# Kernel tuning notes

Hardware: AMD Instinct MI355X
Metric: run time of the kernel (lower is better)

The kernel has to match this reference:

```python
import jax, jax.numpy as jnp
import numpy as np

N_NODES = 50000
N_EDGES = 400000
HID = 128
D_EDGE = 3
D_OUT = 3
LN_EPS = 1e-5


def silu(x):
    return x * jax.nn.sigmoid(x)


def layer_norm(x, gamma, beta):
    mu = jnp.mean(x, axis=-1, keepdims=True)
    var = jnp.mean(jnp.square(x - mu), axis=-1, keepdims=True)
    return (x - mu) * jax.lax.rsqrt(var + LN_EPS) * gamma + beta


def ffn(x, W1, b1, W2, b2, act, gamma=None, beta=None):
    # Linear -> act -> Linear, optional final LayerNorm (FeedForwardBlock)
    h = act(x @ W1 + b1)
    y = h @ W2 + b2
    if gamma is not None:
        y = layer_norm(y, gamma, beta)
    return y


def _mlp_params(key, d_in, d_hid, d_out, use_ln):
    ks = jax.random.split(key, 4)
    p = {
        'W1': jax.random.normal(ks[0], (d_in, d_hid), jnp.float32) / np.sqrt(d_in),
        'b1': jnp.zeros((d_hid,), jnp.float32),
        'W2': jax.random.normal(ks[1], (d_hid, d_out), jnp.float32) / np.sqrt(d_hid),
        'b2': jnp.zeros((d_out,), jnp.float32),
    }
    if use_ln:
        p['g'] = jnp.ones((d_out,), jnp.float32)
        p['be'] = jnp.zeros((d_out,), jnp.float32)
    return p


def setup_inputs() -> dict:
    key = jax.random.key(0)
    ks = jax.random.split(key, 8)
    edge_idx = jax.random.randint(ks[0], (N_EDGES, 2), 0, N_NODES, dtype=jnp.int64)
    edge_features = jax.random.normal(ks[1], (N_EDGES, D_EDGE), jnp.float32)
    node_latents = jax.random.normal(ks[2], (N_NODES, HID), jnp.float32)
    node_features = jax.random.normal(ks[3], (N_NODES, HID), jnp.float32)
    ee = _mlp_params(ks[4], D_EDGE, HID, HID, True)            # embed_edge_fn
    pe = _mlp_params(ks[5], 3 * HID, HID, HID, True)           # process_edge_fn
    pn = _mlp_params(ks[6], 2 * HID, HID, HID, True)           # process_node_fn
    no = _mlp_params(ks[7], HID, HID, D_OUT, False)            # node_output_fn
    inp = {'edge_idx': edge_idx, 'edge_features': edge_features,
           'node_latents': node_latents, 'node_features': node_features}
    for tag, p in (('ee', ee), ('pe', pe), ('pn', pn), ('no', no)):
        for k, v in p.items():
            inp[f'{tag}_{k}'] = v
    return inp


def reference(edge_idx, edge_features, node_latents, node_features,
              ee_W1, ee_b1, ee_W2, ee_b2, ee_g, ee_be,
              pe_W1, pe_b1, pe_W2, pe_b2, pe_g, pe_be,
              pn_W1, pn_b1, pn_W2, pn_b2, pn_g, pn_be,
              no_W1, no_b1, no_W2, no_b2):
    n_nodes = node_features.shape[0]
    senders = edge_idx[:, 0]
    receivers = edge_idx[:, 1]

    # embed raw edge features: [E, D_EDGE] -> [E, HID]
    edge_lat = ffn(edge_features, ee_W1, ee_b1, ee_W2, ee_b2, silu, ee_g, ee_be)

    # edge update: gather sender latents / receiver features, concat-MLP
    sender_f = node_latents[senders]       # [E, HID]
    receiver_f = node_features[receivers]  # [E, HID]
    e_in = jnp.concatenate([sender_f, receiver_f, edge_lat], axis=-1)  # [E, 3*HID]
    new_edge = ffn(e_in, pe_W1, pe_b1, pe_W2, pe_b2, silu, pe_g, pe_be)

    # node update: scatter-mean over receivers, concat-MLP
    seg_sum = jax.ops.segment_sum(new_edge, receivers, num_segments=n_nodes)
    cnt = jax.ops.segment_sum(jnp.ones((new_edge.shape[0], 1), new_edge.dtype),
                              receivers, num_segments=n_nodes)
    mean_edges = seg_sum / jnp.maximum(cnt, 1.0)
    n_in = jnp.concatenate([node_features, mean_edges], axis=-1)  # [N, 2*HID]
    new_node = ffn(n_in, pn_W1, pn_b1, pn_W2, pn_b2, silu, pn_g, pn_be)

    # output head (sigmoid hidden activation, no layer norm)
    out = ffn(new_node, no_W1, no_b1, no_W2, no_b2, jax.nn.sigmoid)
    return (edge_lat, out)
```

## Files before the change

### kernel.cpp

```cpp
#include <hip/hip_runtime.h>


#define N_NODES 50000
#define N_EDGES 400000
#define HID 128
#define LN_EPS 1e-5f

typedef unsigned short u16;
typedef __attribute__((ext_vector_type(8))) short short8;
typedef __attribute__((ext_vector_type(4))) float floatx4;

__device__ __forceinline__ u16 f2bf(float f) {
    union { float f; unsigned int i; } v; v.f = f;
    unsigned int x = v.i;
    return (u16)((x + 0x7FFFu + ((x >> 16) & 1u)) >> 16);
}
__device__ __forceinline__ float bf2f(u16 u) {
    union { unsigned int i; float f; } v; v.i = ((unsigned int)u) << 16;
    return v.f;
}
__device__ __forceinline__ float siluf(float x) { return x * (1.0f / (1.0f + __expf(-x))); }
__device__ __forceinline__ float sigmf(float x) { return 1.0f / (1.0f + __expf(-x)); }

__device__ __forceinline__ short8 pack8(const float* __restrict__ p) {
    union { u16 u[8]; short8 v; } o;
    float4 a = *(const float4*)p;
    float4 b = *(const float4*)(p + 4);
    o.u[0] = f2bf(a.x); o.u[1] = f2bf(a.y); o.u[2] = f2bf(a.z); o.u[3] = f2bf(a.w);
    o.u[4] = f2bf(b.x); o.u[5] = f2bf(b.y); o.u[6] = f2bf(b.z); o.u[7] = f2bf(b.w);
    return o.v;
}
__device__ __forceinline__ short8 pack8s(const float* __restrict__ p, float sc) {
    union { u16 u[8]; short8 v; } o;
    float4 a = *(const float4*)p;
    float4 b = *(const float4*)(p + 4);
    o.u[0] = f2bf(a.x * sc); o.u[1] = f2bf(a.y * sc); o.u[2] = f2bf(a.z * sc); o.u[3] = f2bf(a.w * sc);
    o.u[4] = f2bf(b.x * sc); o.u[5] = f2bf(b.y * sc); o.u[6] = f2bf(b.z * sc); o.u[7] = f2bf(b.w * sc);
    return o.v;
}

__device__ __forceinline__ char* swzp(const void* base, int row, int b) {
    return (char*)base + row * 256 + ((b & 15) | ((((b >> 4) ^ row) & 15) << 4));
}
__device__ __forceinline__ char* swz64(const void* base, int row, int b) {
    return (char*)base + row * 128 + ((b & 15) | ((((b >> 4) ^ row) & 7) << 4));
}

__global__ void k_prepT(const float* __restrict__ src, u16* __restrict__ dst, int K, int N) {
    int i = blockIdx.x * blockDim.x + threadIdx.x;
    if (i < K * N) {
        int k = i / N, n = i - k * N;
        dst[n * K + k] = f2bf(src[i]);
    }
}

__launch_bounds__(256)
__global__ void k_edge_ee(const float* __restrict__ ef,
                          const float* __restrict__ W1, const float* __restrict__ b1v,
                          const u16* __restrict__ W2T, const float* __restrict__ b2v,
                          const float* __restrict__ g, const float* __restrict__ be,
                          float* __restrict__ outEL, u16* __restrict__ elB) {
    __shared__ __align__(16) u16 sW2[128 * 136];
    __shared__ float sW1[384];
    __shared__ float sB1[128];
    const int t = threadIdx.x;
    const int lane = t & 63, w = t >> 6;
    const int l15 = lane & 15, quad = lane >> 4;

    for (int i = t; i < 2048; i += 256) {
        int n = i >> 4, q = i & 15;
        *(uint4*)&sW2[n * 136 + q * 8] = *(const uint4*)&W2T[n * 128 + q * 8];
    }
    for (int i = t; i < 384; i += 256) sW1[i] = W1[i];
    if (t < 128) sB1[t] = b1v[t];
    __syncthreads();

    float b2r[8], gr[8], ber[8];
    #pragma unroll
    for (int nt = 0; nt < 8; ++nt) {
        int col = nt * 16 + l15;
        b2r[nt] = b2v[col]; gr[nt] = g[col]; ber[nt] = be[col];
    }

    for (int tile = blockIdx.x; tile < N_EDGES / 64; tile += gridDim.x) {
        const int e0 = tile * 64;
        const int em = e0 + w * 16 + l15;
        float f0 = ef[em * 3 + 0], f1 = ef[em * 3 + 1], f2 = ef[em * 3 + 2];
        short8 ha[4];
        #pragma unroll
        for (int ks = 0; ks < 4; ++ks) {
            union { u16 u[8]; short8 v; } hh;
            #pragma unroll
            for (int jj = 0; jj < 8; ++jj) {
                int j = ks * 32 + quad * 8 + jj;
                float x = sB1[j] + f0 * sW1[j] + f1 * sW1[128 + j] + f2 * sW1[256 + j];
                hh.u[jj] = f2bf(siluf(x));
            }
            ha[ks] = hh.v;
        }
        floatx4 acc[8];
        #pragma unroll
        for (int nt = 0; nt < 8; ++nt) acc[nt] = (floatx4){0.f, 0.f, 0.f, 0.f};
        #pragma unroll
        for (int ks = 0; ks < 4; ++ks) {
            #pragma unroll
            for (int nt = 0; nt < 8; ++nt) {
                short8 bv = *(const short8*)&sW2[(nt * 16 + l15) * 136 + ks * 32 + quad * 8];
                acc[nt] = __builtin_amdgcn_mfma_f32_16x16x32_bf16(ha[ks], bv, acc[nt], 0, 0, 0);
            }
        }
        float sum[4] = {0, 0, 0, 0}, sq[4] = {0, 0, 0, 0};
        #pragma unroll
        for (int nt = 0; nt < 8; ++nt)
            #pragma unroll
            for (int rr = 0; rr < 4; ++rr) {
                float v = acc[nt][rr] + b2r[nt];
                acc[nt][rr] = v; sum[rr] += v; sq[rr] += v * v;
            }
        #pragma unroll
        for (int m = 1; m < 16; m <<= 1)
            #pragma unroll
            for (int rr = 0; rr < 4; ++rr) {
                sum[rr] += __shfl_xor(sum[rr], m);
                sq[rr]  += __shfl_xor(sq[rr], m);
            }
        float mu[4], rs[4];
        #pragma unroll
        for (int rr = 0; rr < 4; ++rr) {
            mu[rr] = sum[rr] * (1.0f / HID);
            float var = fmaxf(sq[rr] * (1.0f / HID) - mu[rr] * mu[rr], 0.f);
            rs[rr] = rsqrtf(var + LN_EPS);
        }
        #pragma unroll
        for (int nt = 0; nt < 8; ++nt) {
            int col = nt * 16 + l15;
            #pragma unroll
            for (int rr = 0; rr < 4; ++rr) {
                int row = e0 + w * 16 + quad * 4 + rr;
                float v = (acc[nt][rr] - mu[rr]) * rs[rr] * gr[nt] + ber[nt];
                outEL[(size_t)row * HID + col] = v;
                if (elB) elB[(size_t)row * HID + col] = f2bf(v);
            }
        }
    }
}

__launch_bounds__(256)
__global__ void k_gemm128(const float* __restrict__ A, const u16* __restrict__ WT,
                          int ldw, int koff, u16* __restrict__ out) {
    __shared__ __align__(16) u16 sW[128 * 128];
    const int t = threadIdx.x;
    const int lane = t & 63, w = t >> 6;
    const int l15 = lane & 15, quad = lane >> 4;
    for (int i = t; i < 2048; i += 256) {
        int n = i >> 4, q = i & 15;
        *(uint4*)swzp(sW, n, q * 16) = *(const uint4*)&WT[n * ldw + koff + q * 8];
    }
    __syncthreads();
    const int NT = (N_NODES + 63) / 64;
    for (int tile = blockIdx.x; tile < NT; tile += gridDim.x) {
        const int n0 = tile * 64;
        const int arow = n0 + w * 16 + l15;
        const int ac = arow < N_NODES ? arow : 0;
        short8 a[4];
        #pragma unroll
        for (int ks = 0; ks < 4; ++ks)
            a[ks] = pack8(&A[(size_t)ac * HID + ks * 32 + quad * 8]);
        floatx4 acc[8];
        #pragma unroll
        for (int nt = 0; nt < 8; ++nt) acc[nt] = (floatx4){0.f, 0.f, 0.f, 0.f};
        #pragma unroll
        for (int ks = 0; ks < 4; ++ks)
            #pragma unroll
            for (int nt = 0; nt < 8; ++nt) {
                short8 bv = *(const short8*)swzp(sW, nt * 16 + l15, ks * 64 + quad * 16);
                acc[nt] = __builtin_amdgcn_mfma_f32_16x16x32_bf16(a[ks], bv, acc[nt], 0, 0, 0);
            }
        #pragma unroll
        for (int nt = 0; nt < 8; ++nt) {
            #pragma unroll
            for (int rr = 0; rr < 4; ++rr) {
                int orow = n0 + w * 16 + quad * 4 + rr;
                if (orow < N_NODES)
                    out[(size_t)orow * HID + l15 * 8 + nt] = f2bf(acc[nt][rr]);
            }
        }
    }
}

template<bool ELB>
__launch_bounds__(512, 4)
__global__ void k_edge_pe(const int* __restrict__ eidx,
                          const u16* __restrict__ P1, const u16* __restrict__ P2,
                          const float* __restrict__ el, const u16* __restrict__ elB,
                          const u16* __restrict__ W1T, const float* __restrict__ b1v,
                          const u16* __restrict__ W2T, const float* __restrict__ b2v,
                          const float* __restrict__ g, const float* __restrict__ be,
                          float* __restrict__ seg, float* __restrict__ cnt) {
    __shared__ __align__(16) u16 sW1[128 * 128];
    __shared__ __align__(16) u16 sW2[128 * 128];
    __shared__ __align__(16) u16 sH[8][16 * 64];
    const int t = threadIdx.x;
    const int lane = t & 63, w = t >> 6;
    const int l15 = lane & 15, quad = lane >> 4;

    for (int i = t; i < 2048; i += 512) {
        int n = i >> 4, q = i & 15;
        *(uint4*)swzp(sW1, n, q * 16) = *(const uint4*)&W1T[n * 384 + 256 + q * 8];
        *(uint4*)swzp(sW2, n, q * 16) = *(const uint4*)&W2T[n * 128 + q * 8];
    }
    float b1r[8], b2r[8], gr[8], ber[8];
    #pragma unroll
    for (int nt = 0; nt < 8; ++nt) {
        int col = nt * 16 + l15;
        b1r[nt] = b1v[col]; b2r[nt] = b2v[col]; gr[nt] = g[col]; ber[nt] = be[col];
    }
    __syncthreads();

    for (int tile = blockIdx.x; tile < N_EDGES / 128; tile += gridDim.x) {
        const int e0 = tile * 128;
        const int em = e0 + w * 16 + l15;
        int snd[4], rcv[4];
        #pragma unroll
        for (int rr = 0; rr < 4; ++rr) {
            int e = e0 + w * 16 + quad * 4 + rr;
            int2 p = *(const int2*)&eidx[e * 2];
            snd[rr] = p.x; rcv[rr] = p.y;
        }
        floatx4 acc[8];
        #pragma unroll
        for (int rr = 0; rr < 4; ++rr) {
            union { u16 u[8]; short8 v; } p1, p2;
            p1.v = *(const short8*)&P1[(size_t)snd[rr] * HID + l15 * 8];
            p2.v = *(const short8*)&P2[(size_t)rcv[rr] * HID + l15 * 8];
            #pragma unroll
            for (int nt = 0; nt < 8; ++nt)
                acc[nt][rr] = b1r[nt] + bf2f(p1.u[nt]) + bf2f(p2.u[nt]);
        }
        short8 a[4];
        #pragma unroll
        for (int ks = 0; ks < 4; ++ks) {
            if (ELB) a[ks] = *(const short8*)&elB[(size_t)em * HID + ks * 32 + quad * 8];
            else     a[ks] = pack8(&el[(size_t)em * HID + ks * 32 + quad * 8]);
        }
        #pragma unroll
        for (int ks = 0; ks < 4; ++ks)
            #pragma unroll
            for (int nt = 0; nt < 8; ++nt) {
                short8 bv = *(const short8*)swzp(sW1, nt * 16 + l15, ks * 64 + quad * 16);
                acc[nt] = __builtin_amdgcn_mfma_f32_16x16x32_bf16(a[ks], bv, acc[nt], 0, 0, 0);
            }
        short8 ha[4];
        #pragma unroll
        for (int ph = 0; ph < 2; ++ph) {
            #pragma unroll
            for (int n4 = 0; n4 < 4; ++n4) {
                int nt = ph * 4 + n4;
                #pragma unroll
                for (int rr = 0; rr < 4; ++rr)
                    *(u16*)swz64(sH[w], quad * 4 + rr, (n4 * 16 + l15) * 2) =
                        f2bf(siluf(acc[nt][rr]));
            }
            #pragma unroll
            for (int k2 = 0; k2 < 2; ++k2)
                ha[ph * 2 + k2] = *(const short8*)swz64(sH[w], l15, k2 * 64 + quad * 16);
        }
        floatx4 acc2[8];
        #pragma unroll
        for (int nt = 0; nt < 8; ++nt) acc2[nt] = (floatx4){0.f, 0.f, 0.f, 0.f};
        #pragma unroll
        for (int ks = 0; ks < 4; ++ks)
            #pragma unroll
            for (int nt = 0; nt < 8; ++nt) {
                short8 bv = *(const short8*)swzp(sW2, nt * 16 + l15, ks * 64 + quad * 16);
                acc2[nt] = __builtin_amdgcn_mfma_f32_16x16x32_bf16(ha[ks], bv, acc2[nt], 0, 0, 0);
            }
        float sum[4] = {0, 0, 0, 0}, sq[4] = {0, 0, 0, 0};
        #pragma unroll
        for (int nt = 0; nt < 8; ++nt)
            #pragma unroll
            for (int rr = 0; rr < 4; ++rr) {
                float v = acc2[nt][rr] + b2r[nt];
                acc2[nt][rr] = v; sum[rr] += v; sq[rr] += v * v;
            }
        #pragma unroll
        for (int m = 1; m < 16; m <<= 1)
            #pragma unroll
            for (int rr = 0; rr < 4; ++rr) {
                sum[rr] += __shfl_xor(sum[rr], m);
                sq[rr]  += __shfl_xor(sq[rr], m);
            }
        float mu[4], rs[4];
        #pragma unroll
        for (int rr = 0; rr < 4; ++rr) {
            mu[rr] = sum[rr] * (1.0f / HID);
            float var = fmaxf(sq[rr] * (1.0f / HID) - mu[rr] * mu[rr], 0.f);
            rs[rr] = rsqrtf(var + LN_EPS);
        }
        #pragma unroll
        for (int nt = 0; nt < 8; ++nt) {
            int col = nt * 16 + l15;
            #pragma unroll
            for (int rr = 0; rr < 4; ++rr) {
                float v = (acc2[nt][rr] - mu[rr]) * rs[rr] * gr[nt] + ber[nt];
                atomicAdd(&seg[(size_t)rcv[rr] * HID + col], v);
            }
        }
        if (l15 == 0) {
            #pragma unroll
            for (int rr = 0; rr < 4; ++rr) atomicAdd(&cnt[rcv[rr]], 1.0f);
        }
    }
}

__launch_bounds__(512, 4)
__global__ void k_node(const u16* __restrict__ Q1,
                       const float* __restrict__ seg, const float* __restrict__ cnt,
                       const u16* __restrict__ W1T, const float* __restrict__ b1v,
                       const u16* __restrict__ W2T, const float* __restrict__ b2v,
                       const float* __restrict__ g, const float* __restrict__ be,
                       const u16* __restrict__ noW1T, const float* __restrict__ nob1,
                       const float* __restrict__ noW2, const float* __restrict__ nob2,
                       float* __restrict__ outN) {
    __shared__ __align__(16) u16 sW1[128 * 128];
    __shared__ __align__(16) u16 sW2[128 * 128];
    __shared__ __align__(16) u16 sH[8][16 * 64];
    const int t = threadIdx.x;
    const int lane = t & 63, w = t >> 6;
    const int l15 = lane & 15, quad = lane >> 4;

    for (int i = t; i < 2048; i += 512) {
        int n = i >> 4, q = i & 15;
        *(uint4*)swzp(sW1, n, q * 16) = *(const uint4*)&W1T[n * 256 + 128 + q * 8];
        *(uint4*)swzp(sW2, n, q * 16) = *(const uint4*)&W2T[n * 128 + q * 8];
    }
    float b1r[8], b2r[8], gr[8], ber[8], nob1r[8], w2r[8][3];
    #pragma unroll
    for (int nt = 0; nt < 8; ++nt) {
        int col = nt * 16 + l15;
        b1r[nt] = b1v[col]; b2r[nt] = b2v[col]; gr[nt] = g[col]; ber[nt] = be[col];
        nob1r[nt] = nob1[col];
        #pragma unroll
        for (int c = 0; c < 3; ++c) w2r[nt][c] = noW2[col * 3 + c];
    }
    float nob2r[3] = {nob2[0], nob2[1], nob2[2]};
    __syncthreads();

    const int NT = (N_NODES + 127) / 128;
    for (int tile = blockIdx.x; tile < NT; tile += gridDim.x) {
        const int n0 = tile * 128;
        const int node = n0 + w * 16 + l15;
        const int nc = node < N_NODES ? node : 0;
        float inv = 1.0f / fmaxf(cnt[nc], 1.0f);
        short8 a[4];
        #pragma unroll
        for (int ks = 0; ks < 4; ++ks)
            a[ks] = pack8s(&seg[(size_t)nc * HID + ks * 32 + quad * 8], inv);
        floatx4 acc[8];
        int crow[4];
        #pragma unroll
        for (int rr = 0; rr < 4; ++rr) {
            int r = n0 + w * 16 + quad * 4 + rr;
            crow[rr] = r;
            r = r < N_NODES ? r : 0;
            union { u16 u[8]; short8 v; } q1;
            q1.v = *(const short8*)&Q1[(size_t)r * HID + l15 * 8];
            #pragma unroll
            for (int nt = 0; nt < 8; ++nt)
                acc[nt][rr] = b1r[nt] + bf2f(q1.u[nt]);
        }
        #pragma unroll
        for (int ks = 0; ks < 4; ++ks)
            #pragma unroll
            for (int nt = 0; nt < 8; ++nt) {
                short8 bv = *(const short8*)swzp(sW1, nt * 16 + l15, ks * 64 + quad * 16);
                acc[nt] = __builtin_amdgcn_mfma_f32_16x16x32_bf16(a[ks], bv, acc[nt], 0, 0, 0);
            }
        short8 ha[4];
        #pragma unroll
        for (int ph = 0; ph < 2; ++ph) {
            #pragma unroll
            for (int n4 = 0; n4 < 4; ++n4) {
                int nt = ph * 4 + n4;
                #pragma unroll
                for (int rr = 0; rr < 4; ++rr)
                    *(u16*)swz64(sH[w], quad * 4 + rr, (n4 * 16 + l15) * 2) =
                        f2bf(siluf(acc[nt][rr]));
            }
            #pragma unroll
            for (int k2 = 0; k2 < 2; ++k2)
                ha[ph * 2 + k2] = *(const short8*)swz64(sH[w], l15, k2 * 64 + quad * 16);
        }
        floatx4 acc2[8];
        #pragma unroll
        for (int nt = 0; nt < 8; ++nt) acc2[nt] = (floatx4){0.f, 0.f, 0.f, 0.f};
        #pragma unroll
        for (int ks = 0; ks < 4; ++ks)
            #pragma unroll
            for (int nt = 0; nt < 8; ++nt) {
                short8 bv = *(const short8*)swzp(sW2, nt * 16 + l15, ks * 64 + quad * 16);
                acc2[nt] = __builtin_amdgcn_mfma_f32_16x16x32_bf16(ha[ks], bv, acc2[nt], 0, 0, 0);
            }
        float sum[4] = {0, 0, 0, 0}, sq[4] = {0, 0, 0, 0};
        #pragma unroll
        for (int nt = 0; nt < 8; ++nt)
            #pragma unroll
            for (int rr = 0; rr < 4; ++rr) {
                float v = acc2[nt][rr] + b2r[nt];
                acc2[nt][rr] = v; sum[rr] += v; sq[rr] += v * v;
            }
        #pragma unroll
        for (int m = 1; m < 16; m <<= 1)
            #pragma unroll
            for (int rr = 0; rr < 4; ++rr) {
                sum[rr] += __shfl_xor(sum[rr], m);
                sq[rr]  += __shfl_xor(sq[rr], m);
            }
        float mu[4], rs[4];
        #pragma unroll
        for (int rr = 0; rr < 4; ++rr) {
            mu[rr] = sum[rr] * (1.0f / HID);
            float var = fmaxf(sq[rr] * (1.0f / HID) - mu[rr] * mu[rr], 0.f);
            rs[rr] = rsqrtf(var + LN_EPS);
        }
        short8 h2[4];
        #pragma unroll
        for (int ph = 0; ph < 2; ++ph) {
            #pragma unroll
            for (int n4 = 0; n4 < 4; ++n4) {
                int nt = ph * 4 + n4;
                #pragma unroll
                for (int rr = 0; rr < 4; ++rr)
                    *(u16*)swz64(sH[w], quad * 4 + rr, (n4 * 16 + l15) * 2) =
                        f2bf((acc2[nt][rr] - mu[rr]) * rs[rr] * gr[nt] + ber[nt]);
            }
            #pragma unroll
            for (int k2 = 0; k2 < 2; ++k2)
                h2[ph * 2 + k2] = *(const short8*)swz64(sH[w], l15, k2 * 64 + quad * 16);
        }
        floatx4 acc3[8];
        #pragma unroll
        for (int nt = 0; nt < 8; ++nt) acc3[nt] = (floatx4){0.f, 0.f, 0.f, 0.f};
        #pragma unroll
        for (int ks = 0; ks < 4; ++ks)
            #pragma unroll
            for (int nt = 0; nt < 8; ++nt) {
                short8 bv = *(const short8*)&noW1T[(size_t)(nt * 16 + l15) * 128 +
                                                   ks * 32 + quad * 8];
                acc3[nt] = __builtin_amdgcn_mfma_f32_16x16x32_bf16(h2[ks], bv, acc3[nt], 0, 0, 0);
            }
        float p[4][3] = {{0,0,0},{0,0,0},{0,0,0},{0,0,0}};
        #pragma unroll
        for (int nt = 0; nt < 8; ++nt)
            #pragma unroll
            for (int rr = 0; rr < 4; ++rr) {
                float h3 = sigmf(acc3[nt][rr] + nob1r[nt]);
                #pragma unroll
                for (int c = 0; c < 3; ++c) p[rr][c] += h3 * w2r[nt][c];
            }
        #pragma unroll
        for (int m = 1; m < 16; m <<= 1)
            #pragma unroll
            for (int rr = 0; rr < 4; ++rr)
                #pragma unroll
                for (int c = 0; c < 3; ++c) p[rr][c] += __shfl_xor(p[rr][c], m);
        if (l15 < 3) {
            #pragma unroll
            for (int rr = 0; rr < 4; ++rr)
                if (crow[rr] < N_NODES)
                    outN[(size_t)crow[rr] * 3 + l15] = p[rr][l15] + nob2r[l15];
        }
    }
}

extern "C" void kernel_launch(void* const* d_in, const int* in_sizes, int n_in,
                              void* d_out, int out_size, void* d_ws, size_t ws_size,
                              hipStream_t stream) {
    const int*   eidx  = (const int*)d_in[0];
    const float* ef    = (const float*)d_in[1];
    const float* nlat  = (const float*)d_in[2];
    const float* nfeat = (const float*)d_in[3];
    const float* eeW1 = (const float*)d_in[4];
    const float* eeb1 = (const float*)d_in[5];
    const float* eeW2 = (const float*)d_in[6];
    const float* eeb2 = (const float*)d_in[7];
    const float* eeg  = (const float*)d_in[8];
    const float* eebe = (const float*)d_in[9];
    const float* peW1 = (const float*)d_in[10];
    const float* peb1 = (const float*)d_in[11];
    const float* peW2 = (const float*)d_in[12];
    const float* peb2 = (const float*)d_in[13];
    const float* peg  = (const float*)d_in[14];
    const float* pebe = (const float*)d_in[15];
    const float* pnW1 = (const float*)d_in[16];
    const float* pnb1 = (const float*)d_in[17];
    const float* pnW2 = (const float*)d_in[18];
    const float* pnb2 = (const float*)d_in[19];
    const float* png_ = (const float*)d_in[20];
    const float* pnbe = (const float*)d_in[21];
    const float* noW1 = (const float*)d_in[22];
    const float* nob1 = (const float*)d_in[23];
    const float* noW2 = (const float*)d_in[24];
    const float* nob2 = (const float*)d_in[25];

    char* ws = (char*)d_ws;
    float* seg = (float*)ws;
    float* cnt = (float*)(ws + 25600000);
    u16* eeW2T = (u16*)(ws + 25800000);
    u16* peW1T = (u16*)(ws + 25832768);
    u16* peW2T = (u16*)(ws + 25931072);
    u16* pnW1T = (u16*)(ws + 25963840);
    u16* pnW2T = (u16*)(ws + 26029376);
    u16* noW1T = (u16*)(ws + 26062144);
    u16* P1    = (u16*)(ws + 26094912);
    u16* P2    = (u16*)(ws + 38894912);
    const size_t WS_ELB = 51694912 + (size_t)N_EDGES * HID * 2;
    u16* elB = (ws_size >= WS_ELB) ? (u16*)(ws + 51694912) : (u16*)nullptr;

    hipMemsetAsync(ws, 0, 25800000, stream);

    k_prepT<<<64, 256, 0, stream>>>(eeW2, eeW2T, 128, 128);
    k_prepT<<<192, 256, 0, stream>>>(peW1, peW1T, 384, 128);
    k_prepT<<<64, 256, 0, stream>>>(peW2, peW2T, 128, 128);
    k_prepT<<<128, 256, 0, stream>>>(pnW1, pnW1T, 256, 128);
    k_prepT<<<64, 256, 0, stream>>>(pnW2, pnW2T, 128, 128);
    k_prepT<<<64, 256, 0, stream>>>(noW1, noW1T, 128, 128);

    float* outEL = (float*)d_out;
    float* outN  = outEL + (size_t)N_EDGES * HID;

    k_edge_ee<<<1024, 256, 0, stream>>>(ef, eeW1, eeb1, eeW2T, eeb2, eeg, eebe,
                                        outEL, elB);
    k_gemm128<<<512, 256, 0, stream>>>(nlat,  peW1T, 384, 0,   P1);
    k_gemm128<<<512, 256, 0, stream>>>(nfeat, peW1T, 384, 128, P2);
    if (elB)
        k_edge_pe<true><<<512, 512, 0, stream>>>(eidx, P1, P2, outEL, elB, peW1T, peb1,
                                                 peW2T, peb2, peg, pebe, seg, cnt);
    else
        k_edge_pe<false><<<512, 512, 0, stream>>>(eidx, P1, P2, outEL, elB, peW1T, peb1,
                                                  peW2T, peb2, peg, pebe, seg, cnt);
    k_gemm128<<<512, 256, 0, stream>>>(nfeat, pnW1T, 256, 0, P1);
    k_node<<<391, 512, 0, stream>>>(P1, seg, cnt, pnW1T, pnb1, pnW2T, pnb2, png_, pnbe,
                                    noW1T, nob1, noW2, nob2, outN);
}
```

Measured before the change: 773.8 us.

## Replace atomic scatter-mean with CSR gather over bf16 edge outputs

Builds a receiver-sorted CSR index each call (histogram, single-block scan, atomic fill). The edge kernel now writes new edge latents as bf16 via a shared-memory transpose instead of doing float atomics into a node-sized accumulator, and a new per-node kernel gathers and averages them into a bf16 mean. This removes the large memset and the contended float atomics, but adds CSR build kernels, a 100MB edge buffer write and read, and drops the bf16 copy of the edge embedding. k_gemm128 output stores are also vectorised to 16-byte writes.

```diff
diff --git a/kernel.cpp b/kernel.cpp
--- a/kernel.cpp
+++ b/kernel.cpp
@@ -54,12 +54,54 @@
     }
 }
 
+__global__ void k_hist(const int* __restrict__ eidx, int* __restrict__ icnt) {
+    int e = blockIdx.x * blockDim.x + threadIdx.x;
+    if (e < N_EDGES) atomicAdd(&icnt[eidx[e * 2 + 1]], 1);
+}
+
+__launch_bounds__(1024)
+__global__ void k_scan(const int* __restrict__ icnt, int* __restrict__ offs) {
+    __shared__ int s[1024];
+    const int t = threadIdx.x;
+    const int CH = 49;
+    int base = t * CH;
+    int sum = 0;
+    for (int j = 0; j < CH; ++j) {
+        int i = base + j;
+        if (i < N_NODES) sum += icnt[i];
+    }
+    s[t] = sum;
+    __syncthreads();
+    for (int off = 1; off < 1024; off <<= 1) {
+        int v = (t >= off) ? s[t - off] : 0;
+        __syncthreads();
+        s[t] += v;
+        __syncthreads();
+    }
+    int run = s[t] - sum;
+    for (int j = 0; j < CH; ++j) {
+        int i = base + j;
+        if (i < N_NODES) { offs[i] = run; run += icnt[i]; }
+    }
+    if (t == 1023) offs[N_NODES] = s[1023];
+}
+
+__global__ void k_fill(const int* __restrict__ eidx, const int* __restrict__ offs,
+                       int* __restrict__ fpos, int* __restrict__ csr) {
+    int e = blockIdx.x * blockDim.x + threadIdx.x;
+    if (e < N_EDGES) {
+        int r = eidx[e * 2 + 1];
+        int p = atomicAdd(&fpos[r], 1);
+        csr[offs[r] + p] = e;
+    }
+}
+
 __launch_bounds__(256)
 __global__ void k_edge_ee(const float* __restrict__ ef,
                           const float* __restrict__ W1, const float* __restrict__ b1v,
                           const u16* __restrict__ W2T, const float* __restrict__ b2v,
                           const float* __restrict__ g, const float* __restrict__ be,
-                          float* __restrict__ outEL, u16* __restrict__ elB) {
+                          float* __restrict__ outEL) {
     __shared__ __align__(16) u16 sW2[128 * 136];
     __shared__ float sW1[384];
     __shared__ float sB1[128];
@@ -137,9 +179,7 @@
             #pragma unroll
             for (int rr = 0; rr < 4; ++rr) {
                 int row = e0 + w * 16 + quad * 4 + rr;
-                float v = (acc[nt][rr] - mu[rr]) * rs[rr] * gr[nt] + ber[nt];
-                outEL[(size_t)row * HID + col] = v;
-                if (elB) elB[(size_t)row * HID + col] = f2bf(v);
+                outEL[(size_t)row * HID + col] = (acc[nt][rr] - mu[rr]) * rs[rr] * gr[nt] + ber[nt];
             }
         }
     }
@@ -177,25 +217,26 @@
                 acc[nt] = __builtin_amdgcn_mfma_f32_16x16x32_bf16(a[ks], bv, acc[nt], 0, 0, 0);
             }
         #pragma unroll
-        for (int nt = 0; nt < 8; ++nt) {
-            #pragma unroll
-            for (int rr = 0; rr < 4; ++rr) {
-                int orow = n0 + w * 16 + quad * 4 + rr;
-                if (orow < N_NODES)
-                    out[(size_t)orow * HID + l15 * 8 + nt] = f2bf(acc[nt][rr]);
-            }
-        }
-    }
-}
-
-template<bool ELB>
+        for (int rr = 0; rr < 4; ++rr) {
+            int orow = n0 + w * 16 + quad * 4 + rr;
+            union { u16 u[8]; short8 v; } o;
+            #pragma unroll
+            for (int nt = 0; nt < 8; ++nt) o.u[nt] = f2bf(acc[nt][rr]);
+            if (orow < N_NODES)
+                *(short8*)&out[(size_t)orow * HID + l15 * 8] = o.v;
+        }
+    }
+}
+
+template<bool CSR>
 __launch_bounds__(512, 4)
 __global__ void k_edge_pe(const int* __restrict__ eidx,
                           const u16* __restrict__ P1, const u16* __restrict__ P2,
-                          const float* __restrict__ el, const u16* __restrict__ elB,
+                          const float* __restrict__ el,
                           const u16* __restrict__ W1T, const float* __restrict__ b1v,
                           const u16* __restrict__ W2T, const float* __restrict__ b2v,
                           const float* __restrict__ g, const float* __restrict__ be,
+                          u16* __restrict__ newE,
                           float* __restrict__ seg, float* __restrict__ cnt) {
     __shared__ __align__(16) u16 sW1[128 * 128];
     __shared__ __align__(16) u16 sW2[128 * 128];
@@ -239,10 +280,8 @@
         }
         short8 a[4];
         #pragma unroll
-        for (int ks = 0; ks < 4; ++ks) {
-            if (ELB) a[ks] = *(const short8*)&elB[(size_t)em * HID + ks * 32 + quad * 8];
-            else     a[ks] = pack8(&el[(size_t)em * HID + ks * 32 + quad * 8]);
-        }
+        for (int ks = 0; ks < 4; ++ks)
+            a[ks] = pack8(&el[(size_t)em * HID + ks * 32 + quad * 8]);
         #pragma unroll
         for (int ks = 0; ks < 4; ++ks)
             #pragma unroll
@@ -297,24 +336,66 @@
             float var = fmaxf(sq[rr] * (1.0f / HID) - mu[rr] * mu[rr], 0.f);
             rs[rr] = rsqrtf(var + LN_EPS);
         }
-        #pragma unroll
-        for (int nt = 0; nt < 8; ++nt) {
-            int col = nt * 16 + l15;
-            #pragma unroll
-            for (int rr = 0; rr < 4; ++rr) {
-                float v = (acc2[nt][rr] - mu[rr]) * rs[rr] * gr[nt] + ber[nt];
-                atomicAdd(&seg[(size_t)rcv[rr] * HID + col], v);
-            }
-        }
-        if (l15 == 0) {
-            #pragma unroll
-            for (int rr = 0; rr < 4; ++rr) atomicAdd(&cnt[rcv[rr]], 1.0f);
-        }
-    }
-}
-
+        if (CSR) {
+            #pragma unroll
+            for (int ph = 0; ph < 2; ++ph) {
+                #pragma unroll
+                for (int n4 = 0; n4 < 4; ++n4) {
+                    int nt = ph * 4 + n4;
+                    #pragma unroll
+                    for (int rr = 0; rr < 4; ++rr)
+                        *(u16*)swz64(sH[w], quad * 4 + rr, (n4 * 16 + l15) * 2) =
+                            f2bf((acc2[nt][rr] - mu[rr]) * rs[rr] * gr[nt] + ber[nt]);
+                }
+                #pragma unroll
+                for (int k2 = 0; k2 < 2; ++k2) {
+                    short8 row = *(const short8*)swz64(sH[w], l15, k2 * 64 + quad * 16);
+                    *(short8*)&newE[(size_t)em * HID + ph * 64 + k2 * 32 + quad * 8] = row;
+                }
+            }
+        } else {
+            #pragma unroll
+            for (int nt = 0; nt < 8; ++nt) {
+                int col = nt * 16 + l15;
+                #pragma unroll
+                for (int rr = 0; rr < 4; ++rr) {
+                    float v = (acc2[nt][rr] - mu[rr]) * rs[rr] * gr[nt] + ber[nt];
+                    atomicAdd(&seg[(size_t)rcv[rr] * HID + col], v);
+                }
+            }
+            if (l15 == 0) {
+                #pragma unroll
+                for (int rr = 0; rr < 4; ++rr) atomicAdd(&cnt[rcv[rr]], 1.0f);
+            }
+        }
+    }
+}
+
+__launch_bounds__(256)
+__global__ void k_mean(const u16* __restrict__ newE, const int* __restrict__ offs,
+                       const int* __restrict__ csr, u16* __restrict__ meanB) {
+    const int wid = (int)((blockIdx.x * blockDim.x + threadIdx.x) >> 6);
+    const int lane = threadIdx.x & 63;
+    const int nW = (int)((gridDim.x * blockDim.x) >> 6);
+    for (int n = wid; n < N_NODES; n += nW) {
+        int s0 = offs[n], s1 = offs[n + 1];
+        float a0 = 0.f, a1 = 0.f;
+        for (int d = s0; d < s1; ++d) {
+            int e = csr[d];
+            unsigned int v = *(const unsigned int*)&newE[(size_t)e * HID + lane * 2];
+            a0 += bf2f((u16)(v & 0xFFFFu));
+            a1 += bf2f((u16)(v >> 16));
+        }
+        int deg = s1 - s0;
+        float inv = 1.0f / (float)(deg > 0 ? deg : 1);
+        unsigned int o = (unsigned int)f2bf(a0 * inv) | (((unsigned int)f2bf(a1 * inv)) << 16);
+        *(unsigned int*)&meanB[(size_t)n * HID + lane * 2] = o;
+    }
+}
+
+template<bool CSR>
 __launch_bounds__(512, 4)
-__global__ void k_node(const u16* __restrict__ Q1,
+__global__ void k_node(const u16* __restrict__ Q1, const u16* __restrict__ meanB,
                        const float* __restrict__ seg, const float* __restrict__ cnt,
                        const u16* __restrict__ W1T, const float* __restrict__ b1v,
                        const u16* __restrict__ W2T, const float* __restrict__ b2v,
@@ -351,11 +432,17 @@
         const int n0 = tile * 128;
         const int node = n0 + w * 16 + l15;
         const int nc = node < N_NODES ? node : 0;
-        float inv = 1.0f / fmaxf(cnt[nc], 1.0f);
         short8 a[4];
-        #pragma unroll
-        for (int ks = 0; ks < 4; ++ks)
-            a[ks] = pack8s(&seg[(size_t)nc * HID + ks * 32 + quad * 8], inv);
+        if (CSR) {
+            #pragma unroll
+            for (int ks = 0; ks < 4; ++ks)
+                a[ks] = *(const short8*)&meanB[(size_t)nc * HID + ks * 32 + quad * 8];
+        } else {
+            float inv = 1.0f / fmaxf(cnt[nc], 1.0f);
+            #pragma unroll
+            for (int ks = 0; ks < 4; ++ks)
+                a[ks] = pack8s(&seg[(size_t)nc * HID + ks * 32 + quad * 8], inv);
+        }
         floatx4 acc[8];
         int crow[4];
         #pragma unroll
@@ -503,43 +590,84 @@
     const float* noW2 = (const float*)d_in[24];
     const float* nob2 = (const float*)d_in[25];
 
-    char* ws = (char*)d_ws;
-    float* seg = (float*)ws;
-    float* cnt = (float*)(ws + 25600000);
-    u16* eeW2T = (u16*)(ws + 25800000);
-    u16* peW1T = (u16*)(ws + 25832768);
-    u16* peW2T = (u16*)(ws + 25931072);
-    u16* pnW1T = (u16*)(ws + 25963840);
-    u16* pnW2T = (u16*)(ws + 26029376);
-    u16* noW1T = (u16*)(ws + 26062144);
-    u16* P1    = (u16*)(ws + 26094912);
-    u16* P2    = (u16*)(ws + 38894912);
-    const size_t WS_ELB = 51694912 + (size_t)N_EDGES * HID * 2;
-    u16* elB = (ws_size >= WS_ELB) ? (u16*)(ws + 51694912) : (u16*)nullptr;
-
-    hipMemsetAsync(ws, 0, 25800000, stream);
-
-    k_prepT<<<64, 256, 0, stream>>>(eeW2, eeW2T, 128, 128);
-    k_prepT<<<192, 256, 0, stream>>>(peW1, peW1T, 384, 128);
-    k_prepT<<<64, 256, 0, stream>>>(peW2, peW2T, 128, 128);
-    k_prepT<<<128, 256, 0, stream>>>(pnW1, pnW1T, 256, 128);
-    k_prepT<<<64, 256, 0, stream>>>(pnW2, pnW2T, 128, 128);
-    k_prepT<<<64, 256, 0, stream>>>(noW1, noW1T, 128, 128);
-
     float* outEL = (float*)d_out;
     float* outN  = outEL + (size_t)N_EDGES * HID;
-
-    k_edge_ee<<<1024, 256, 0, stream>>>(ef, eeW1, eeb1, eeW2T, eeb2, eeg, eebe,
-                                        outEL, elB);
-    k_gemm128<<<512, 256, 0, stream>>>(nlat,  peW1T, 384, 0,   P1);
-    k_gemm128<<<512, 256, 0, stream>>>(nfeat, peW1T, 384, 128, P2);
-    if (elB)
-        k_edge_pe<true><<<512, 512, 0, stream>>>(eidx, P1, P2, outEL, elB, peW1T, peb1,
-                                                 peW2T, peb2, peg, pebe, seg, cnt);
-    else
-        k_edge_pe<false><<<512, 512, 0, stream>>>(eidx, P1, P2, outEL, elB, peW1T, peb1,
-                                                  peW2T, peb2, peg, pebe, seg, cnt);
-    k_gemm128<<<512, 256, 0, stream>>>(nfeat, pnW1T, 256, 0, P1);
-    k_node<<<391, 512, 0, stream>>>(P1, seg, cnt, pnW1T, pnb1, pnW2T, pnb2, png_, pnbe,
-                                    noW1T, nob1, noW2, nob2, outN);
-}
+    char* ws = (char*)d_ws;
+
+    const size_t WS_CSR = 130494928;
+    const bool useCSR = ws_size >= WS_CSR;
+
+    u16 *eeW2T, *peW1T, *peW2T, *pnW1T, *pnW2T, *noW1T, *P1, *P2;
+    if (useCSR) {
+        eeW2T = (u16*)(ws + 0);
+        peW1T = (u16*)(ws + 32768);
+        peW2T = (u16*)(ws + 131072);
+        pnW1T = (u16*)(ws + 163840);
+        pnW2T = (u16*)(ws + 229376);
+        noW1T = (u16*)(ws + 262144);
+        int* icnt = (int*)(ws + 294912);
+        int* offs = (int*)(ws + 494912);
+        int* fpos = (int*)(ws + 694916);
+        int* csr  = (int*)(ws + 894916);
+        P1 = (u16*)(ws + 2494928);
+        P2 = (u16*)(ws + 15294928);
+        u16* newE  = (u16*)(ws + 28094928);
+        u16* meanB = P2;
+
+        hipMemsetAsync(ws + 294912, 0, 600004, stream);
+
+        k_prepT<<<64, 256, 0, stream>>>(eeW2, eeW2T, 128, 128);
+        k_prepT<<<192, 256, 0, stream>>>(peW1, peW1T, 384, 128);
+        k_prepT<<<64, 256, 0, stream>>>(peW2, peW2T, 128, 128);
+        k_prepT<<<128, 256, 0, stream>>>(pnW1, pnW1T, 256, 128);
+        k_prepT<<<64, 256, 0, stream>>>(pnW2, pnW2T, 128, 128);
+        k_prepT<<<64, 256, 0, stream>>>(noW1, noW1T, 128, 128);
+
+        k_hist<<<782, 512, 0, stream>>>(eidx, icnt);
+        k_scan<<<1, 1024, 0, stream>>>(icnt, offs);
+        k_fill<<<782, 512, 0, stream>>>(eidx, offs, fpos, csr);
+
+        k_edge_ee<<<1024, 256, 0, stream>>>(ef, eeW1, eeb1, eeW2T, eeb2, eeg, eebe, outEL);
+        k_gemm128<<<512, 256, 0, stream>>>(nlat,  peW1T, 384, 0,   P1);
+        k_gemm128<<<512, 256, 0, stream>>>(nfeat, peW1T, 384, 128, P2);
+        k_edge_pe<true><<<512, 512, 0, stream>>>(eidx, P1, P2, outEL, peW1T, peb1,
+                                                 peW2T, peb2, peg, pebe, newE,
+                                                 (float*)nullptr, (float*)nullptr);
+        k_mean<<<1024, 256, 0, stream>>>(newE, offs, csr, meanB);
+        k_gemm128<<<512, 256, 0, stream>>>(nfeat, pnW1T, 256, 0, P1);
+        k_node<true><<<391, 512, 0, stream>>>(P1, meanB, (float*)nullptr, (float*)nullptr,
+                                              pnW1T, pnb1, pnW2T, pnb2, png_, pnbe,
+                                              noW1T, nob1, noW2, nob2, outN);
+    } else {
+        float* seg = (float*)ws;
+        float* cnt = (float*)(ws + 25600000);
+        eeW2T = (u16*)(ws + 25800000);
+        peW1T = (u16*)(ws + 25832768);
+        peW2T = (u16*)(ws + 25931072);
+        pnW1T = (u16*)(ws + 25963840);
+        pnW2T = (u16*)(ws + 26029376);
+        noW1T = (u16*)(ws + 26062144);
+        P1    = (u16*)(ws + 26094912);
+        P2    = (u16*)(ws + 38894912);
+
+        hipMemsetAsync(ws, 0, 25800000, stream);
+
+        k_prepT<<<64, 256, 0, stream>>>(eeW2, eeW2T, 128, 128);
+        k_prepT<<<192, 256, 0, stream>>>(peW1, peW1T, 384, 128);
+        k_prepT<<<64, 256, 0, stream>>>(peW2, peW2T, 128, 128);
+        k_prepT<<<128, 256, 0, stream>>>(pnW1, pnW1T, 256, 128);
+        k_prepT<<<64, 256, 0, stream>>>(pnW2, pnW2T, 128, 128);
+        k_prepT<<<64, 256, 0, stream>>>(noW1, noW1T, 128, 128);
+
+        k_edge_ee<<<1024, 256, 0, stream>>>(ef, eeW1, eeb1, eeW2T, eeb2, eeg, eebe, outEL);
+        k_gemm128<<<512, 256, 0, stream>>>(nlat,  peW1T, 384, 0,   P1);
+        k_gemm128<<<512, 256, 0, stream>>>(nfeat, peW1T, 384, 128, P2);
+        k_edge_pe<false><<<512, 512, 0, stream>>>(eidx, P1, P2, outEL, peW1T, peb1,
+                                                  peW2T, peb2, peg, pebe, (u16*)nullptr,
+                                                  seg, cnt);
+        k_gemm128<<<512, 256, 0, stream>>>(nfeat, pnW1T, 256, 0, P1);
+        k_node<false><<<391, 512, 0, stream>>>(P1, (u16*)nullptr, seg, cnt,
+                                               pnW1T, pnb1, pnW2T, pnb2, png_, pnbe,
+                                               noW1T, nob1, noW2, nob2, outN);
+    }
+}
```

Result: slower. 1.043 ms (+34.7%).

## Replace atomic scatter-mean with CSR-by-receiver per-node edge processing

Applied to the files above, without the earlier changes.

Builds a receiver-sorted CSR (histogram, single-block scan, fill) and processes edges grouped per destination node, one wave per node, so the segment mean is reduced in registers and written once as bf16. This removes the 128 float atomics per edge, the large seg/cnt memset, and the fp32 seg re-read in the node kernel. The cost is three extra small kernels, a serial one-block scan, and partly-filled 16-row MFMA tiles for low-degree nodes (average degree about 8), which roughly doubles the MFMA work for the edge MLP. The bf16 edge-latent copy is dropped, and gathers of edge latents become random rather than contiguous.

```diff
diff --git a/kernel.cpp b/kernel.cpp
--- a/kernel.cpp
+++ b/kernel.cpp
@@ -30,14 +30,6 @@
     o.u[4] = f2bf(b.x); o.u[5] = f2bf(b.y); o.u[6] = f2bf(b.z); o.u[7] = f2bf(b.w);
     return o.v;
 }
-__device__ __forceinline__ short8 pack8s(const float* __restrict__ p, float sc) {
-    union { u16 u[8]; short8 v; } o;
-    float4 a = *(const float4*)p;
-    float4 b = *(const float4*)(p + 4);
-    o.u[0] = f2bf(a.x * sc); o.u[1] = f2bf(a.y * sc); o.u[2] = f2bf(a.z * sc); o.u[3] = f2bf(a.w * sc);
-    o.u[4] = f2bf(b.x * sc); o.u[5] = f2bf(b.y * sc); o.u[6] = f2bf(b.z * sc); o.u[7] = f2bf(b.w * sc);
-    return o.v;
-}
 
 __device__ __forceinline__ char* swzp(const void* base, int row, int b) {
     return (char*)base + row * 256 + ((b & 15) | ((((b >> 4) ^ row) & 15) << 4));
@@ -54,12 +46,55 @@
     }
 }
 
+__global__ void k_hist(const int* __restrict__ eidx, int* __restrict__ icnt) {
+    int e = blockIdx.x * blockDim.x + threadIdx.x;
+    if (e < N_EDGES) atomicAdd(&icnt[eidx[e * 2 + 1]], 1);
+}
+
+__launch_bounds__(1024)
+__global__ void k_scan(const int* __restrict__ icnt, int* __restrict__ offs) {
+    __shared__ int s[1024];
+    const int t = threadIdx.x;
+    const int CH = 49;
+    int base = t * CH;
+    int sum = 0;
+    for (int j = 0; j < CH; ++j) {
+        int i = base + j;
+        if (i < N_NODES) sum += icnt[i];
+    }
+    s[t] = sum;
+    __syncthreads();
+    for (int off = 1; off < 1024; off <<= 1) {
+        int v = (t >= off) ? s[t - off] : 0;
+        __syncthreads();
+        s[t] += v;
+        __syncthreads();
+    }
+    int run = s[t] - sum;
+    for (int j = 0; j < CH; ++j) {
+        int i = base + j;
+        if (i < N_NODES) { offs[i] = run; run += icnt[i]; }
+    }
+    if (t == 1023) offs[N_NODES] = s[1023];
+}
+
+__global__ void k_fill(const int* __restrict__ eidx, const int* __restrict__ offs,
+                       int* __restrict__ fpos, int2* __restrict__ csrES) {
+    int e = blockIdx.x * blockDim.x + threadIdx.x;
+    if (e < N_EDGES) {
+        int2 pr = *(const int2*)&eidx[e * 2];
+        int p = atomicAdd(&fpos[pr.y], 1);
+        int2 es; es.x = e; es.y = pr.x;
+        csrES[offs[pr.y] + p] = es;
+    }
+}
+
 __launch_bounds__(256)
 __global__ void k_edge_ee(const float* __restrict__ ef,
                           const float* __restrict__ W1, const float* __restrict__ b1v,
                           const u16* __restrict__ W2T, const float* __restrict__ b2v,
                           const float* __restrict__ g, const float* __restrict__ be,
-                          float* __restrict__ outEL, u16* __restrict__ elB) {
+                          float* __restrict__ outEL) {
     __shared__ __align__(16) u16 sW2[128 * 136];
     __shared__ float sW1[384];
     __shared__ float sB1[128];
@@ -137,9 +172,7 @@
             #pragma unroll
             for (int rr = 0; rr < 4; ++rr) {
                 int row = e0 + w * 16 + quad * 4 + rr;
-                float v = (acc[nt][rr] - mu[rr]) * rs[rr] * gr[nt] + ber[nt];
-                outEL[(size_t)row * HID + col] = v;
-                if (elB) elB[(size_t)row * HID + col] = f2bf(v);
+                outEL[(size_t)row * HID + col] = (acc[nt][rr] - mu[rr]) * rs[rr] * gr[nt] + ber[nt];
             }
         }
     }
@@ -177,34 +210,33 @@
                 acc[nt] = __builtin_amdgcn_mfma_f32_16x16x32_bf16(a[ks], bv, acc[nt], 0, 0, 0);
             }
         #pragma unroll
-        for (int nt = 0; nt < 8; ++nt) {
-            #pragma unroll
-            for (int rr = 0; rr < 4; ++rr) {
-                int orow = n0 + w * 16 + quad * 4 + rr;
-                if (orow < N_NODES)
-                    out[(size_t)orow * HID + l15 * 8 + nt] = f2bf(acc[nt][rr]);
-            }
-        }
-    }
-}
-
-template<bool ELB>
-__launch_bounds__(512, 4)
-__global__ void k_edge_pe(const int* __restrict__ eidx,
+        for (int rr = 0; rr < 4; ++rr) {
+            int orow = n0 + w * 16 + quad * 4 + rr;
+            union { u16 u[8]; short8 v; } o;
+            #pragma unroll
+            for (int nt = 0; nt < 8; ++nt) o.u[nt] = f2bf(acc[nt][rr]);
+            if (orow < N_NODES)
+                *(short8*)&out[(size_t)orow * HID + l15 * 8] = o.v;
+        }
+    }
+}
+
+__launch_bounds__(256)
+__global__ void k_pe_node(const int2* __restrict__ csrES, const int* __restrict__ offs,
                           const u16* __restrict__ P1, const u16* __restrict__ P2,
-                          const float* __restrict__ el, const u16* __restrict__ elB,
+                          const float* __restrict__ el,
                           const u16* __restrict__ W1T, const float* __restrict__ b1v,
                           const u16* __restrict__ W2T, const float* __restrict__ b2v,
                           const float* __restrict__ g, const float* __restrict__ be,
-                          float* __restrict__ seg, float* __restrict__ cnt) {
+                          u16* __restrict__ meanB) {
     __shared__ __align__(16) u16 sW1[128 * 128];
     __shared__ __align__(16) u16 sW2[128 * 128];
-    __shared__ __align__(16) u16 sH[8][16 * 64];
+    __shared__ __align__(16) u16 sH[4][16 * 64];
     const int t = threadIdx.x;
     const int lane = t & 63, w = t >> 6;
     const int l15 = lane & 15, quad = lane >> 4;
 
-    for (int i = t; i < 2048; i += 512) {
+    for (int i = t; i < 2048; i += 256) {
         int n = i >> 4, q = i & 15;
         *(uint4*)swzp(sW1, n, q * 16) = *(const uint4*)&W1T[n * 384 + 256 + q * 8];
         *(uint4*)swzp(sW2, n, q * 16) = *(const uint4*)&W2T[n * 128 + q * 8];
@@ -217,105 +249,115 @@
     }
     __syncthreads();
 
-    for (int tile = blockIdx.x; tile < N_EDGES / 128; tile += gridDim.x) {
-        const int e0 = tile * 128;
-        const int em = e0 + w * 16 + l15;
-        int snd[4], rcv[4];
-        #pragma unroll
-        for (int rr = 0; rr < 4; ++rr) {
-            int e = e0 + w * 16 + quad * 4 + rr;
-            int2 p = *(const int2*)&eidx[e * 2];
-            snd[rr] = p.x; rcv[rr] = p.y;
-        }
-        floatx4 acc[8];
-        #pragma unroll
-        for (int rr = 0; rr < 4; ++rr) {
-            union { u16 u[8]; short8 v; } p1, p2;
-            p1.v = *(const short8*)&P1[(size_t)snd[rr] * HID + l15 * 8];
-            p2.v = *(const short8*)&P2[(size_t)rcv[rr] * HID + l15 * 8];
+    const int nW = (int)((gridDim.x * blockDim.x) >> 6);
+    const int wid = (int)((blockIdx.x * blockDim.x + threadIdx.x) >> 6);
+
+    for (int n = wid; n < N_NODES; n += nW) {
+        const int s0 = offs[n], s1 = offs[n + 1];
+        const int deg = s1 - s0;
+        float msum[8];
+        #pragma unroll
+        for (int nt = 0; nt < 8; ++nt) msum[nt] = 0.f;
+        union { u16 u[8]; short8 v; } p2r;
+        p2r.v = *(const short8*)&P2[(size_t)n * HID + l15 * 8];
+
+        for (int c0 = s0; c0 < s1; c0 += 16) {
+            int nv = s1 - c0; if (nv > 16) nv = 16;
+            int2 es = csrES[c0 + (l15 < nv ? l15 : nv - 1)];
+            short8 a[4];
+            #pragma unroll
+            for (int ks = 0; ks < 4; ++ks)
+                a[ks] = pack8(&el[(size_t)es.x * HID + ks * 32 + quad * 8]);
+            floatx4 acc[8];
+            #pragma unroll
+            for (int rr = 0; rr < 4; ++rr) {
+                int sndr = __shfl(es.y, quad * 4 + rr);
+                union { u16 u[8]; short8 v; } p1r;
+                p1r.v = *(const short8*)&P1[(size_t)sndr * HID + l15 * 8];
+                #pragma unroll
+                for (int nt = 0; nt < 8; ++nt)
+                    acc[nt][rr] = b1r[nt] + bf2f(p1r.u[nt]) + bf2f(p2r.u[nt]);
+            }
+            #pragma unroll
+            for (int ks = 0; ks < 4; ++ks)
+                #pragma unroll
+                for (int nt = 0; nt < 8; ++nt) {
+                    short8 bv = *(const short8*)swzp(sW1, nt * 16 + l15, ks * 64 + quad * 16);
+                    acc[nt] = __builtin_amdgcn_mfma_f32_16x16x32_bf16(a[ks], bv, acc[nt], 0, 0, 0);
+                }
+            short8 ha[4];
+            #pragma unroll
+            for (int ph = 0; ph < 2; ++ph) {
+                #pragma unroll
+                for (int n4 = 0; n4 < 4; ++n4) {
+                    int nt = ph * 4 + n4;
+                    #pragma unroll
+                    for (int rr = 0; rr < 4; ++rr)
+                        *(u16*)swz64(sH[w], quad * 4 + rr, (n4 * 16 + l15) * 2) =
+                            f2bf(siluf(acc[nt][rr]));
+                }
+                #pragma unroll
+                for (int k2 = 0; k2 < 2; ++k2)
+                    ha[ph * 2 + k2] = *(const short8*)swz64(sH[w], l15, k2 * 64 + quad * 16);
+            }
+            floatx4 acc2[8];
+            #pragma unroll
+            for (int nt = 0; nt < 8; ++nt) acc2[nt] = (floatx4){0.f, 0.f, 0.f, 0.f};
+            #pragma unroll
+            for (int ks = 0; ks < 4; ++ks)
+                #pragma unroll
+                for (int nt = 0; nt < 8; ++nt) {
+                    short8 bv = *(const short8*)swzp(sW2, nt * 16 + l15, ks * 64 + quad * 16);
+                    acc2[nt] = __builtin_amdgcn_mfma_f32_16x16x32_bf16(ha[ks], bv, acc2[nt], 0, 0, 0);
+                }
+            float sum[4] = {0, 0, 0, 0}, sq[4] = {0, 0, 0, 0};
             #pragma unroll
             for (int nt = 0; nt < 8; ++nt)
-                acc[nt][rr] = b1r[nt] + bf2f(p1.u[nt]) + bf2f(p2.u[nt]);
-        }
-        short8 a[4];
-        #pragma unroll
-        for (int ks = 0; ks < 4; ++ks) {
-            if (ELB) a[ks] = *(const short8*)&elB[(size_t)em * HID + ks * 32 + quad * 8];
-            else     a[ks] = pack8(&el[(size_t)em * HID + ks * 32 + quad * 8]);
-        }
-        #pragma unroll
-        for (int ks = 0; ks < 4; ++ks)
+                #pragma unroll
+                for (int rr = 0; rr < 4; ++rr) {
+                    float v = acc2[nt][rr] + b2r[nt];
+                    acc2[nt][rr] = v; sum[rr] += v; sq[rr] += v * v;
+                }
+            #pragma unroll
+            for (int m = 1; m < 16; m <<= 1)
+                #pragma unroll
+                for (int rr = 0; rr < 4; ++rr) {
+                    sum[rr] += __shfl_xor(sum[rr], m);
+                    sq[rr]  += __shfl_xor(sq[rr], m);
+                }
+            float mu[4], rs[4];
+            #pragma unroll
+            for (int rr = 0; rr < 4; ++rr) {
+                mu[rr] = sum[rr] * (1.0f / HID);
+                float var = fmaxf(sq[rr] * (1.0f / HID) - mu[rr] * mu[rr], 0.f);
+                rs[rr] = rsqrtf(var + LN_EPS);
+            }
             #pragma unroll
             for (int nt = 0; nt < 8; ++nt) {
-                short8 bv = *(const short8*)swzp(sW1, nt * 16 + l15, ks * 64 + quad * 16);
-                acc[nt] = __builtin_amdgcn_mfma_f32_16x16x32_bf16(a[ks], bv, acc[nt], 0, 0, 0);
-            }
-        short8 ha[4];
-        #pragma unroll
-        for (int ph = 0; ph < 2; ++ph) {
-            #pragma unroll
-            for (int n4 = 0; n4 < 4; ++n4) {
-                int nt = ph * 4 + n4;
-                #pragma unroll
-                for (int rr = 0; rr < 4; ++rr)
-                    *(u16*)swz64(sH[w], quad * 4 + rr, (n4 * 16 + l15) * 2) =
-                        f2bf(siluf(acc[nt][rr]));
-            }
-            #pragma unroll
-            for (int k2 = 0; k2 < 2; ++k2)
-                ha[ph * 2 + k2] = *(const short8*)swz64(sH[w], l15, k2 * 64 + quad * 16);
-        }
-        floatx4 acc2[8];
-        #pragma unroll
-        for (int nt = 0; nt < 8; ++nt) acc2[nt] = (floatx4){0.f, 0.f, 0.f, 0.f};
-        #pragma unroll
-        for (int ks = 0; ks < 4; ++ks)
-            #pragma unroll
-            for (int nt = 0; nt < 8; ++nt) {
-                short8 bv = *(const short8*)swzp(sW2, nt * 16 + l15, ks * 64 + quad * 16);
-                acc2[nt] = __builtin_amdgcn_mfma_f32_16x16x32_bf16(ha[ks], bv, acc2[nt], 0, 0, 0);
-            }
-        float sum[4] = {0, 0, 0, 0}, sq[4] = {0, 0, 0, 0};
-        #pragma unroll
-        for (int nt = 0; nt < 8; ++nt)
-            #pragma unroll
-            for (int rr = 0; rr < 4; ++rr) {
-                float v = acc2[nt][rr] + b2r[nt];
-                acc2[nt][rr] = v; sum[rr] += v; sq[rr] += v * v;
-            }
-        #pragma unroll
-        for (int m = 1; m < 16; m <<= 1)
-            #pragma unroll
-            for (int rr = 0; rr < 4; ++rr) {
-                sum[rr] += __shfl_xor(sum[rr], m);
-                sq[rr]  += __shfl_xor(sq[rr], m);
-            }
-        float mu[4], rs[4];
-        #pragma unroll
-        for (int rr = 0; rr < 4; ++rr) {
-            mu[rr] = sum[rr] * (1.0f / HID);
-            float var = fmaxf(sq[rr] * (1.0f / HID) - mu[rr] * mu[rr], 0.f);
-            rs[rr] = rsqrtf(var + LN_EPS);
-        }
-        #pragma unroll
-        for (int nt = 0; nt < 8; ++nt) {
-            int col = nt * 16 + l15;
-            #pragma unroll
-            for (int rr = 0; rr < 4; ++rr) {
-                float v = (acc2[nt][rr] - mu[rr]) * rs[rr] * gr[nt] + ber[nt];
-                atomicAdd(&seg[(size_t)rcv[rr] * HID + col], v);
-            }
-        }
-        if (l15 == 0) {
-            #pragma unroll
-            for (int rr = 0; rr < 4; ++rr) atomicAdd(&cnt[rcv[rr]], 1.0f);
-        }
+                float s = 0.f;
+                #pragma unroll
+                for (int rr = 0; rr < 4; ++rr) {
+                    float v = (acc2[nt][rr] - mu[rr]) * rs[rr] * gr[nt] + ber[nt];
+                    if (quad * 4 + rr < nv) s += v;
+                }
+                s += __shfl_xor(s, 16);
+                s += __shfl_xor(s, 32);
+                msum[nt] += s;
+            }
+        }
+        float inv = 1.0f / (float)(deg > 0 ? deg : 1);
+        u16* sm = (u16*)sH[w];
+        if (quad == 0) {
+            #pragma unroll
+            for (int nt = 0; nt < 8; ++nt) sm[nt * 16 + l15] = f2bf(msum[nt] * inv);
+        }
+        if (quad == 0)
+            *(short8*)&meanB[(size_t)n * HID + l15 * 8] = *(const short8*)&sm[l15 * 8];
     }
 }
 
 __launch_bounds__(512, 4)
-__global__ void k_node(const u16* __restrict__ Q1,
-                       const float* __restrict__ seg, const float* __restrict__ cnt,
+__global__ void k_node(const u16* __restrict__ Q1, const u16* __restrict__ meanB,
                        const u16* __restrict__ W1T, const float* __restrict__ b1v,
                        const u16* __restrict__ W2T, const float* __restrict__ b2v,
                        const float* __restrict__ g, const float* __restrict__ be,
@@ -351,11 +393,10 @@
         const int n0 = tile * 128;
         const int node = n0 + w * 16 + l15;
         const int nc = node < N_NODES ? node : 0;
-        float inv = 1.0f / fmaxf(cnt[nc], 1.0f);
         short8 a[4];
         #pragma unroll
         for (int ks = 0; ks < 4; ++ks)
-            a[ks] = pack8s(&seg[(size_t)nc * HID + ks * 32 + quad * 8], inv);
+            a[ks] = *(const short8*)&meanB[(size_t)nc * HID + ks * 32 + quad * 8];
         floatx4 acc[8];
         int crow[4];
         #pragma unroll
@@ -503,21 +544,25 @@
     const float* noW2 = (const float*)d_in[24];
     const float* nob2 = (const float*)d_in[25];
 
+    float* outEL = (float*)d_out;
+    float* outN  = outEL + (size_t)N_EDGES * HID;
     char* ws = (char*)d_ws;
-    float* seg = (float*)ws;
-    float* cnt = (float*)(ws + 25600000);
-    u16* eeW2T = (u16*)(ws + 25800000);
-    u16* peW1T = (u16*)(ws + 25832768);
-    u16* peW2T = (u16*)(ws + 25931072);
-    u16* pnW1T = (u16*)(ws + 25963840);
-    u16* pnW2T = (u16*)(ws + 26029376);
-    u16* noW1T = (u16*)(ws + 26062144);
-    u16* P1    = (u16*)(ws + 26094912);
-    u16* P2    = (u16*)(ws + 38894912);
-    const size_t WS_ELB = 51694912 + (size_t)N_EDGES * HID * 2;
-    u16* elB = (ws_size >= WS_ELB) ? (u16*)(ws + 51694912) : (u16*)nullptr;
-
-    hipMemsetAsync(ws, 0, 25800000, stream);
+
+    u16*  eeW2T = (u16*)(ws + 0);
+    u16*  peW1T = (u16*)(ws + 32768);
+    u16*  peW2T = (u16*)(ws + 131072);
+    u16*  pnW1T = (u16*)(ws + 163840);
+    u16*  pnW2T = (u16*)(ws + 229376);
+    u16*  noW1T = (u16*)(ws + 262144);
+    int*  icnt  = (int*)(ws + 294912);
+    int*  offs  = (int*)(ws + 494912);
+    int*  fpos  = (int*)(ws + 694920);
+    int2* csrES = (int2*)(ws + 894920);
+    u16*  P1    = (u16*)(ws + 4096000);
+    u16*  P2    = (u16*)(ws + 16896000);
+    u16*  meanB = (u16*)(ws + 29696000);
+
+    hipMemsetAsync(ws + 294912, 0, 600008, stream);
 
     k_prepT<<<64, 256, 0, stream>>>(eeW2, eeW2T, 128, 128);
     k_prepT<<<192, 256, 0, stream>>>(peW1, peW1T, 384, 128);
@@ -526,20 +571,18 @@
     k_prepT<<<64, 256, 0, stream>>>(pnW2, pnW2T, 128, 128);
     k_prepT<<<64, 256, 0, stream>>>(noW1, noW1T, 128, 128);
 
-    float* outEL = (float*)d_out;
-    float* outN  = outEL + (size_t)N_EDGES * HID;
-
-    k_edge_ee<<<1024, 256, 0, stream>>>(ef, eeW1, eeb1, eeW2T, eeb2, eeg, eebe,
-                                        outEL, elB);
+    k_hist<<<782, 512, 0, stream>>>(eidx, icnt);
+    k_scan<<<1, 1024, 0, stream>>>(icnt, offs);
+    k_fill<<<782, 512, 0, stream>>>(eidx, offs, fpos, csrES);
+
+    k_edge_ee<<<1024, 256, 0, stream>>>(ef, eeW1, eeb1, eeW2T, eeb2, eeg, eebe, outEL);
     k_gemm128<<<512, 256, 0, stream>>>(nlat,  peW1T, 384, 0,   P1);
     k_gemm128<<<512, 256, 0, stream>>>(nfeat, peW1T, 384, 128, P2);
-    if (elB)
-        k_edge_pe<true><<<512, 512, 0, stream>>>(eidx, P1, P2, outEL, elB, peW1T, peb1,
-                                                 peW2T, peb2, peg, pebe, seg, cnt);
-    else
-        k_edge_pe<false><<<512, 512, 0, stream>>>(eidx, P1, P2, outEL, elB, peW1T, peb1,
-                                                  peW2T, peb2, peg, pebe, seg, cnt);
+
+    k_pe_node<<<1024, 256, 0, stream>>>(csrES, offs, P1, P2, outEL, peW1T, peb1,
+                                        peW2T, peb2, peg, pebe, meanB);
+
     k_gemm128<<<512, 256, 0, stream>>>(nfeat, pnW1T, 256, 0, P1);
-    k_node<<<391, 512, 0, stream>>>(P1, seg, cnt, pnW1T, pnb1, pnW2T, pnb2, png_, pnbe,
+    k_node<<<391, 512, 0, stream>>>(P1, meanB, pnW1T, pnb1, pnW2T, pnb2, png_, pnbe,
                                     noW1T, nob1, noW2, nob2, outN);
 }
```

Measured after the change: 1.030 ms. +33.2%, slower.
